# Kernel optimization log

Measured on AMD Instinct MI355X. Metric: run time of the kernel, lower is better.

## Reference

```python
import jax, jax.numpy as jnp
import numpy as np

N = 50000      # nodes
DEG = 16       # avg degree
E = N * DEG    # edges
FIN = 128
FQK = 64
FV = 64
H = 8


def setup_inputs() -> dict:
    key = jax.random.key(0)
    k1, k2, k3, k4 = jax.random.split(key, 4)
    x = jax.random.normal(k1, (N, FIN), dtype=jnp.float32)
    # torch Linear(Fin, 2*Fqk+Fv, bias=False); stored here as [Fin, Ftot] so y = x @ W
    W = jax.random.normal(k2, (FIN, 2 * FQK + FV), dtype=jnp.float32) / np.sqrt(FIN)
    # edges: src sorted and covering all nodes (required by scatter_softmax semantics)
    src = jnp.repeat(jnp.arange(N, dtype=jnp.int32), DEG)
    dest = jax.random.randint(k3, (E,), 0, N, dtype=jnp.int32)
    ei = jnp.stack([src, dest])  # [2, E]
    batch = jnp.sort(jax.random.randint(k4, (N,), 0, 64, dtype=jnp.int32))
    return {"x": x, "W": W, "batch": batch, "ei": ei}


def reference(x, W, batch, ei):
    n = x.shape[0]
    Fh = FQK // H   # per-head qk dim
    Fhv = FV // H   # per-head v dim
    scaling = float(Fh) ** (-0.5)

    qkv = x @ W  # [N, 2*Fqk+Fv]
    q, k, v = jnp.split(qkv, [FQK, 2 * FQK], axis=-1)
    q = (q * scaling).reshape(n, H, Fh)
    k = k.reshape(n, H, Fh)
    v = v.reshape(n, H, Fhv)

    src, dest = ei[0], ei[1]
    qs = q[src]   # [E, H, Fh]
    ks = k[dest]  # [E, H, Fh]
    vs = v[dest]  # [E, H, Fhv]

    aw = jnp.einsum("ehf,ehf->eh", qs, ks)  # per-edge per-head logits

    # segment softmax over src (numerically stable, same math as exp/segsum(exp))
    amax = jax.ops.segment_max(aw, src, num_segments=n)
    ex = jnp.exp(aw - amax[src])
    denom = jax.ops.segment_sum(ex, src, num_segments=n)
    aw = ex / denom[src]  # [E, H]

    out = jax.ops.segment_sum(aw[:, :, None] * vs, src, num_segments=n)  # [N, H, Fhv]
    return out.reshape(n, H * Fhv)
```

## Files before the change

### kernel.cpp

```cpp
#include <hip/hip_runtime.h>
#include <math.h>

#define N_NODES 50000
#define DEG 16
#define E_EDGES (N_NODES * DEG)
#define FIN 128
#define FTOT 192
#define FQK 64
#define FV 64
#define H 8

typedef __attribute__((ext_vector_type(8))) short short8;
typedef __attribute__((ext_vector_type(4))) float float4v;

__device__ inline unsigned short f2bf(float f) {
    unsigned int u = __float_as_uint(f);
    unsigned int r = u + 0x7fffu + ((u >> 16) & 1u);
    return (unsigned short)(r >> 16);
}

#define LDC 194

__global__ __launch_bounds__(256) void wprep(const float* __restrict__ W,
                                             unsigned short* __restrict__ Wb) {
    const int t = blockIdx.x * 256 + threadIdx.x;
    const int n = t % 192, kg = t / 192;
    unsigned short tmp[8];
#pragma unroll
    for (int j = 0; j < 8; j++)
        tmp[j] = f2bf(W[(kg * 8 + j) * FTOT + n]);
    *(uint4*)(Wb + n * FIN + kg * 8) = *(const uint4*)tmp;
}

__global__ __launch_bounds__(256) void gemm_qkv(const float* __restrict__ x,
                                                const unsigned short* __restrict__ Wb,
                                                unsigned short* __restrict__ qkv) {
    __shared__ unsigned short Bt[FTOT * FIN];
    unsigned short* Ct = Bt;
    const int tid = threadIdx.x;
    const int wave = tid >> 6, lane = tid & 63;
    const int m = lane & 15, q = lane >> 4;
    const int row = blockIdx.x * 64 + wave * 16 + m;
    const int rowc = min(row, N_NODES - 1);

    short8 a[4];
    const float* xr = x + (size_t)rowc * FIN;
#pragma unroll
    for (int s = 0; s < 4; s++) {
        float4v f0 = *(const float4v*)(xr + s * 32 + q * 8);
        float4v f1 = *(const float4v*)(xr + s * 32 + q * 8 + 4);
        short8 av;
        av[0] = (short)f2bf(f0.x); av[1] = (short)f2bf(f0.y);
        av[2] = (short)f2bf(f0.z); av[3] = (short)f2bf(f0.w);
        av[4] = (short)f2bf(f1.x); av[5] = (short)f2bf(f1.y);
        av[6] = (short)f2bf(f1.z); av[7] = (short)f2bf(f1.w);
        a[s] = av;
    }

#pragma unroll
    for (int i = 0; i < 12; i++) {
        const int c = i * 256 + tid;
        uint4 v = *(const uint4*)(Wb + c * 8);
        const int cs = c ^ ((c >> 4) & 7);
        *(uint4*)(&Bt[cs * 8]) = v;
    }
    __syncthreads();

    float4v acc[12];
#pragma unroll
    for (int ct = 0; ct < 12; ct++) acc[ct] = (float4v){0.f, 0.f, 0.f, 0.f};
#pragma unroll
    for (int ct = 0; ct < 12; ct++) {
        const int n = ct * 16 + m;
        const int sw = (n & 7) << 4;
#pragma unroll
        for (int s = 0; s < 4; s++) {
            const short8 b = *(const short8*)((const char*)Bt +
                             (((n << 8) + s * 64 + q * 16) ^ sw));
            acc[ct] = __builtin_amdgcn_mfma_f32_16x16x32_bf16(a[s], b, acc[ct], 0, 0, 0);
        }
    }
    __syncthreads();

    const int lrow0 = wave * 16 + q * 4;
#pragma unroll
    for (int ct = 0; ct < 12; ct++) {
        const int col = ct * 16 + m;
        int off; float scale;
        if (col < FQK)          { off = col;                      scale = 0.35355339059327373f; }
        else if (col < 2 * FQK) { off = 64 + 2 * (col - 64);      scale = 1.f; }
        else                    { off = 64 + 2 * (col - 128) + 1; scale = 1.f; }
#pragma unroll
        for (int i = 0; i < 4; i++)
            Ct[(lrow0 + i) * LDC + off] = f2bf(acc[ct][i] * scale);
    }
    __syncthreads();

    unsigned int* qg = (unsigned int*)qkv;
    const int base = blockIdx.x * 64;
#pragma unroll
    for (int i = 0; i < 24; i++) {
        int l = tid + i * 256;
        int r = l / 96, dw = l - r * 96;
        if (base + r < N_NODES)
            qg[(size_t)(base + r) * 96 + dw] = *(const unsigned int*)(&Ct[r * LDC + 2 * dw]);
    }
}

__global__ __launch_bounds__(256) void attn(const unsigned short* __restrict__ qkv,
                                            const int* __restrict__ dest,
                                            float* __restrict__ out) {
    const int node = blockIdx.x * 4 + (threadIdx.x >> 6);
    const int lane = threadIdx.x & 63;
    const int g = lane >> 2;
    const int r = lane & 3;
    if (node >= N_NODES) return;

    const int d = dest[node * DEG + g];

    const unsigned short* qp = qkv + (size_t)node * FTOT + 16 * r;
    const uint4 qv0 = *(const uint4*)(qp);
    const uint4 qv1 = *(const uint4*)(qp + 8);

    const unsigned short* kp = qkv + (size_t)d * FTOT + 64 + 32 * r;
    const uint4 kv0 = *(const uint4*)(kp);
    const uint4 kv1 = *(const uint4*)(kp + 8);
    const uint4 kv2 = *(const uint4*)(kp + 16);
    const uint4 kv3 = *(const uint4*)(kp + 24);

    const unsigned int qw[8]  = {qv0.x, qv0.y, qv0.z, qv0.w, qv1.x, qv1.y, qv1.z, qv1.w};
    const unsigned int kvw[16] = {kv0.x, kv0.y, kv0.z, kv0.w, kv1.x, kv1.y, kv1.z, kv1.w,
                                  kv2.x, kv2.y, kv2.z, kv2.w, kv3.x, kv3.y, kv3.z, kv3.w};

    float la = 0.f, lb = 0.f;
#pragma unroll
    for (int f = 0; f < 8; f++) {
        const unsigned int qa = qw[f >> 1];
        const unsigned int qb = qw[(f + 8) >> 1];
        const float qfa = __uint_as_float((f & 1) ? (qa & 0xffff0000u) : (qa << 16));
        const float qfb = __uint_as_float((f & 1) ? (qb & 0xffff0000u) : (qb << 16));
        la = fmaf(qfa, __uint_as_float(kvw[f] << 16), la);
        lb = fmaf(qfb, __uint_as_float(kvw[f + 8] << 16), lb);
    }

    float ma = la, mb = lb;
    ma = fmaxf(ma, __shfl_xor(ma, 4, 64));  mb = fmaxf(mb, __shfl_xor(mb, 4, 64));
    ma = fmaxf(ma, __shfl_xor(ma, 8, 64));  mb = fmaxf(mb, __shfl_xor(mb, 8, 64));
    ma = fmaxf(ma, __shfl_xor(ma, 16, 64)); mb = fmaxf(mb, __shfl_xor(mb, 16, 64));
    ma = fmaxf(ma, __shfl_xor(ma, 32, 64)); mb = fmaxf(mb, __shfl_xor(mb, 32, 64));
    const float pa = __expf(la - ma);
    const float pb = __expf(lb - mb);
    float sa = pa, sb = pb;
    sa += __shfl_xor(sa, 4, 64);  sb += __shfl_xor(sb, 4, 64);
    sa += __shfl_xor(sa, 8, 64);  sb += __shfl_xor(sb, 8, 64);
    sa += __shfl_xor(sa, 16, 64); sb += __shfl_xor(sb, 16, 64);
    sa += __shfl_xor(sa, 32, 64); sb += __shfl_xor(sb, 32, 64);

    float o[16];
#pragma unroll
    for (int w = 0; w < 8; w++) {
        o[w]     = pa * __uint_as_float(kvw[w] & 0xffff0000u);
        o[w + 8] = pb * __uint_as_float(kvw[w + 8] & 0xffff0000u);
    }
    {
        const bool up = (lane & 4) != 0;
#pragma unroll
        for (int j = 0; j < 8; j++) {
            const float send = up ? o[j] : o[j + 8];
            const float recv = __shfl_xor(send, 4, 64);
            o[j] = (up ? o[j + 8] : o[j]) + recv;
        }
    }
    {
        const bool up = (lane & 8) != 0;
#pragma unroll
        for (int j = 0; j < 4; j++) {
            const float send = up ? o[j] : o[j + 4];
            const float recv = __shfl_xor(send, 8, 64);
            o[j] = (up ? o[j + 4] : o[j]) + recv;
        }
    }
    {
        const bool up = (lane & 16) != 0;
#pragma unroll
        for (int j = 0; j < 2; j++) {
            const float send = up ? o[j] : o[j + 2];
            const float recv = __shfl_xor(send, 16, 64);
            o[j] = (up ? o[j + 2] : o[j]) + recv;
        }
    }
    {
        const bool up = (lane & 32) != 0;
        const float send = up ? o[0] : o[1];
        const float recv = __shfl_xor(send, 32, 64);
        o[0] = (up ? o[1] : o[0]) + recv;
    }
    const int w = ((g & 1) << 3) | ((g & 2) << 1) | ((g & 4) >> 1) | ((g & 8) >> 3);
    out[(size_t)node * 64 + 16 * r + w] = o[0] / ((w < 8) ? sa : sb);
}

extern "C" void kernel_launch(void* const* d_in, const int* in_sizes, int n_in,
                              void* d_out, int out_size, void* d_ws, size_t ws_size,
                              hipStream_t stream) {
    const float* x = (const float*)d_in[0];
    const float* W = (const float*)d_in[1];
    const int* ei = (const int*)d_in[3];
    const int* dest = ei + E_EDGES;
    float* out = (float*)d_out;

    unsigned short* qkv = (unsigned short*)d_ws;
    unsigned short* Wb  = qkv + (size_t)N_NODES * FTOT;

    wprep<<<12, 256, 0, stream>>>(W, Wb);
    gemm_qkv<<<(N_NODES + 63) / 64, 256, 0, stream>>>(x, Wb, qkv);
    attn<<<(N_NODES + 3) / 4, 256, 0, stream>>>(qkv, dest, out);
}
```

Before: 113.2 us.

## Fuse weight prep, QKV GEMM and attention into one persistent kernel with grid barrier

Merges the three kernels into one launch of 782 blocks. Each block converts W to bf16 in two halves directly into a smaller LDS buffer, computes its 64-row QKV tile, then waits at a global atomic barrier before running attention over 64 nodes per block with software prefetch of the next node's dest index and q. This removes two launch gaps and the separate W-prep pass, and cuts LDS use so more blocks fit per CU. The cost is that every block redoes the W conversion from fp32 global memory, and a spin barrier that relies on all 782 blocks being resident at once.

```diff
diff --git a/kernel.cpp b/kernel.cpp
--- a/kernel.cpp
+++ b/kernel.cpp
@@ -9,6 +9,7 @@
 #define FQK 64
 #define FV 64
 #define H 8
+#define NBLK 782
 
 typedef __attribute__((ext_vector_type(8))) short short8;
 typedef __attribute__((ext_vector_type(4))) float float4v;
@@ -21,182 +22,206 @@
 
 #define LDC 194
 
-__global__ __launch_bounds__(256) void wprep(const float* __restrict__ W,
-                                             unsigned short* __restrict__ Wb) {
-    const int t = blockIdx.x * 256 + threadIdx.x;
-    const int n = t % 192, kg = t / 192;
-    unsigned short tmp[8];
-#pragma unroll
-    for (int j = 0; j < 8; j++)
-        tmp[j] = f2bf(W[(kg * 8 + j) * FTOT + n]);
-    *(uint4*)(Wb + n * FIN + kg * 8) = *(const uint4*)tmp;
-}
-
-__global__ __launch_bounds__(256) void gemm_qkv(const float* __restrict__ x,
-                                                const unsigned short* __restrict__ Wb,
-                                                unsigned short* __restrict__ qkv) {
-    __shared__ unsigned short Bt[FTOT * FIN];
-    unsigned short* Ct = Bt;
+__global__ __launch_bounds__(256, 4) void fused(const float* __restrict__ x,
+                                                const float* __restrict__ W,
+                                                const int* __restrict__ dest,
+                                                unsigned short* __restrict__ qkv,
+                                                unsigned int* __restrict__ bar,
+                                                float* __restrict__ out) {
+    __shared__ unsigned short Bt[12544];
     const int tid = threadIdx.x;
     const int wave = tid >> 6, lane = tid & 63;
-    const int m = lane & 15, q = lane >> 4;
-    const int row = blockIdx.x * 64 + wave * 16 + m;
-    const int rowc = min(row, N_NODES - 1);
-
-    short8 a[4];
-    const float* xr = x + (size_t)rowc * FIN;
-#pragma unroll
-    for (int s = 0; s < 4; s++) {
-        float4v f0 = *(const float4v*)(xr + s * 32 + q * 8);
-        float4v f1 = *(const float4v*)(xr + s * 32 + q * 8 + 4);
-        short8 av;
-        av[0] = (short)f2bf(f0.x); av[1] = (short)f2bf(f0.y);
-        av[2] = (short)f2bf(f0.z); av[3] = (short)f2bf(f0.w);
-        av[4] = (short)f2bf(f1.x); av[5] = (short)f2bf(f1.y);
-        av[6] = (short)f2bf(f1.z); av[7] = (short)f2bf(f1.w);
-        a[s] = av;
+
+    {
+        const int m = lane & 15, q = lane >> 4;
+        const int row = blockIdx.x * 64 + wave * 16 + m;
+        const int rowc = min(row, N_NODES - 1);
+
+        short8 a[4];
+        const float* xr = x + (size_t)rowc * FIN;
+#pragma unroll
+        for (int s = 0; s < 4; s++) {
+            float4v f0 = *(const float4v*)(xr + s * 32 + q * 8);
+            float4v f1 = *(const float4v*)(xr + s * 32 + q * 8 + 4);
+            short8 av;
+            av[0] = (short)f2bf(f0.x); av[1] = (short)f2bf(f0.y);
+            av[2] = (short)f2bf(f0.z); av[3] = (short)f2bf(f0.w);
+            av[4] = (short)f2bf(f1.x); av[5] = (short)f2bf(f1.y);
+            av[6] = (short)f2bf(f1.z); av[7] = (short)f2bf(f1.w);
+            a[s] = av;
+        }
+
+        float4v acc[12];
+#pragma unroll
+        for (int ct = 0; ct < 12; ct++) acc[ct] = (float4v){0.f, 0.f, 0.f, 0.f};
+
+#pragma unroll
+        for (int h = 0; h < 2; h++) {
+#pragma unroll
+            for (int i = 0; i < 6; i++) {
+                const int c = i * 256 + tid;
+                const int n = c % 96, kg = c / 96;
+                unsigned short tmp[8];
+#pragma unroll
+                for (int j = 0; j < 8; j++)
+                    tmp[j] = f2bf(W[(kg * 8 + j) * FTOT + h * 96 + n]);
+                const int cs = (n * 16 + kg) ^ (n & 7);
+                *(uint4*)(&Bt[cs * 8]) = *(const uint4*)tmp;
+            }
+            __syncthreads();
+#pragma unroll
+            for (int j = 0; j < 6; j++) {
+                const int nl = j * 16 + m;
+                const int sw = (nl & 7) << 4;
+#pragma unroll
+                for (int s = 0; s < 4; s++) {
+                    const short8 b = *(const short8*)((const char*)Bt +
+                                     (((nl << 8) + s * 64 + q * 16) ^ sw));
+                    acc[h * 6 + j] =
+                        __builtin_amdgcn_mfma_f32_16x16x32_bf16(a[s], b, acc[h * 6 + j], 0, 0, 0);
+                }
+            }
+            __syncthreads();
+        }
+
+        unsigned short* Ct = Bt;
+        const int lrow0 = wave * 16 + q * 4;
+#pragma unroll
+        for (int ct = 0; ct < 12; ct++) {
+            const int col = ct * 16 + m;
+            int off; float scale;
+            if (col < FQK)          { off = col;                      scale = 0.35355339059327373f; }
+            else if (col < 2 * FQK) { off = 64 + 2 * (col - 64);      scale = 1.f; }
+            else                    { off = 64 + 2 * (col - 128) + 1; scale = 1.f; }
+#pragma unroll
+            for (int i = 0; i < 4; i++)
+                Ct[(lrow0 + i) * LDC + off] = f2bf(acc[ct][i] * scale);
+        }
+        __syncthreads();
+
+        unsigned int* qg = (unsigned int*)qkv;
+        const int base = blockIdx.x * 64;
+#pragma unroll
+        for (int i = 0; i < 24; i++) {
+            int l = tid + i * 256;
+            int r = l / 96, dw = l - r * 96;
+            if (base + r < N_NODES)
+                qg[(size_t)(base + r) * 96 + dw] = *(const unsigned int*)(&Ct[r * LDC + 2 * dw]);
+        }
     }
 
-#pragma unroll
-    for (int i = 0; i < 12; i++) {
-        const int c = i * 256 + tid;
-        uint4 v = *(const uint4*)(Wb + c * 8);
-        const int cs = c ^ ((c >> 4) & 7);
-        *(uint4*)(&Bt[cs * 8]) = v;
+    __threadfence();
+    if (tid == 0) {
+        __hip_atomic_fetch_add(bar, 1u, __ATOMIC_RELAXED, __HIP_MEMORY_SCOPE_AGENT);
+        while (__hip_atomic_load(bar, __ATOMIC_RELAXED, __HIP_MEMORY_SCOPE_AGENT) < NBLK)
+            __builtin_amdgcn_s_sleep(1);
     }
     __syncthreads();
-
-    float4v acc[12];
-#pragma unroll
-    for (int ct = 0; ct < 12; ct++) acc[ct] = (float4v){0.f, 0.f, 0.f, 0.f};
-#pragma unroll
-    for (int ct = 0; ct < 12; ct++) {
-        const int n = ct * 16 + m;
-        const int sw = (n & 7) << 4;
-#pragma unroll
-        for (int s = 0; s < 4; s++) {
-            const short8 b = *(const short8*)((const char*)Bt +
-                             (((n << 8) + s * 64 + q * 16) ^ sw));
-            acc[ct] = __builtin_amdgcn_mfma_f32_16x16x32_bf16(a[s], b, acc[ct], 0, 0, 0);
+    __threadfence();
+
+    {
+        const int g = lane >> 2;
+        const int r = lane & 3;
+        int node = blockIdx.x * 64 + wave;
+
+        int nodec = min(node, N_NODES - 1);
+        int d = dest[nodec * DEG + g];
+        const unsigned short* qp0 = qkv + (size_t)nodec * FTOT + 16 * r;
+        uint4 qv0 = *(const uint4*)(qp0);
+        uint4 qv1 = *(const uint4*)(qp0 + 8);
+
+#pragma unroll 1
+        for (int t = 0; t < 16; ++t) {
+            const unsigned short* kp = qkv + (size_t)d * FTOT + 64 + 32 * r;
+            const uint4 kv0 = *(const uint4*)(kp);
+            const uint4 kv1 = *(const uint4*)(kp + 8);
+            const uint4 kv2 = *(const uint4*)(kp + 16);
+            const uint4 kv3 = *(const uint4*)(kp + 24);
+
+            const int noden = node + 4;
+            int dN = d; uint4 nq0 = qv0, nq1 = qv1;
+            if (t < 15) {
+                const int nc = min(noden, N_NODES - 1);
+                dN = dest[nc * DEG + g];
+                const unsigned short* nqp = qkv + (size_t)nc * FTOT + 16 * r;
+                nq0 = *(const uint4*)(nqp);
+                nq1 = *(const uint4*)(nqp + 8);
+            }
+
+            const unsigned int qw[8]  = {qv0.x, qv0.y, qv0.z, qv0.w, qv1.x, qv1.y, qv1.z, qv1.w};
+            const unsigned int kvw[16] = {kv0.x, kv0.y, kv0.z, kv0.w, kv1.x, kv1.y, kv1.z, kv1.w,
+                                          kv2.x, kv2.y, kv2.z, kv2.w, kv3.x, kv3.y, kv3.z, kv3.w};
+
+            float la = 0.f, lb = 0.f;
+#pragma unroll
+            for (int f = 0; f < 8; f++) {
+                const unsigned int qa = qw[f >> 1];
+                const unsigned int qb = qw[(f + 8) >> 1];
+                const float qfa = __uint_as_float((f & 1) ? (qa & 0xffff0000u) : (qa << 16));
+                const float qfb = __uint_as_float((f & 1) ? (qb & 0xffff0000u) : (qb << 16));
+                la = fmaf(qfa, __uint_as_float(kvw[f] << 16), la);
+                lb = fmaf(qfb, __uint_as_float(kvw[f + 8] << 16), lb);
+            }
+
+            float ma = la, mb = lb;
+            ma = fmaxf(ma, __shfl_xor(ma, 4, 64));  mb = fmaxf(mb, __shfl_xor(mb, 4, 64));
+            ma = fmaxf(ma, __shfl_xor(ma, 8, 64));  mb = fmaxf(mb, __shfl_xor(mb, 8, 64));
+            ma = fmaxf(ma, __shfl_xor(ma, 16, 64)); mb = fmaxf(mb, __shfl_xor(mb, 16, 64));
+            ma = fmaxf(ma, __shfl_xor(ma, 32, 64)); mb = fmaxf(mb, __shfl_xor(mb, 32, 64));
+            const float pa = __expf(la - ma);
+            const float pb = __expf(lb - mb);
+            float sa = pa, sb = pb;
+            sa += __shfl_xor(sa, 4, 64);  sb += __shfl_xor(sb, 4, 64);
+            sa += __shfl_xor(sa, 8, 64);  sb += __shfl_xor(sb, 8, 64);
+            sa += __shfl_xor(sa, 16, 64); sb += __shfl_xor(sb, 16, 64);
+            sa += __shfl_xor(sa, 32, 64); sb += __shfl_xor(sb, 32, 64);
+
+            float o[16];
+#pragma unroll
+            for (int w = 0; w < 8; w++) {
+                o[w]     = pa * __uint_as_float(kvw[w] & 0xffff0000u);
+                o[w + 8] = pb * __uint_as_float(kvw[w + 8] & 0xffff0000u);
+            }
+            {
+                const bool up = (lane & 4) != 0;
+#pragma unroll
+                for (int j = 0; j < 8; j++) {
+                    const float send = up ? o[j] : o[j + 8];
+                    const float recv = __shfl_xor(send, 4, 64);
+                    o[j] = (up ? o[j + 8] : o[j]) + recv;
+                }
+            }
+            {
+                const bool up = (lane & 8) != 0;
+#pragma unroll
+                for (int j = 0; j < 4; j++) {
+                    const float send = up ? o[j] : o[j + 4];
+                    const float recv = __shfl_xor(send, 8, 64);
+                    o[j] = (up ? o[j + 4] : o[j]) + recv;
+                }
+            }
+            {
+                const bool up = (lane & 16) != 0;
+#pragma unroll
+                for (int j = 0; j < 2; j++) {
+                    const float send = up ? o[j] : o[j + 2];
+                    const float recv = __shfl_xor(send, 16, 64);
+                    o[j] = (up ? o[j + 2] : o[j]) + recv;
+                }
+            }
+            {
+                const bool up = (lane & 32) != 0;
+                const float send = up ? o[0] : o[1];
+                const float recv = __shfl_xor(send, 32, 64);
+                o[0] = (up ? o[1] : o[0]) + recv;
+            }
+            const int w = ((g & 1) << 3) | ((g & 2) << 1) | ((g & 4) >> 1) | ((g & 8) >> 3);
+            if (node < N_NODES)
+                out[(size_t)node * 64 + 16 * r + w] = o[0] / ((w < 8) ? sa : sb);
+
+            node = noden; d = dN; qv0 = nq0; qv1 = nq1;
         }
     }
-    __syncthreads();
-
-    const int lrow0 = wave * 16 + q * 4;
-#pragma unroll
-    for (int ct = 0; ct < 12; ct++) {
-        const int col = ct * 16 + m;
-        int off; float scale;
-        if (col < FQK)          { off = col;                      scale = 0.35355339059327373f; }
-        else if (col < 2 * FQK) { off = 64 + 2 * (col - 64);      scale = 1.f; }
-        else                    { off = 64 + 2 * (col - 128) + 1; scale = 1.f; }
-#pragma unroll
-        for (int i = 0; i < 4; i++)
-            Ct[(lrow0 + i) * LDC + off] = f2bf(acc[ct][i] * scale);
-    }
-    __syncthreads();
-
-    unsigned int* qg = (unsigned int*)qkv;
-    const int base = blockIdx.x * 64;
-#pragma unroll
-    for (int i = 0; i < 24; i++) {
-        int l = tid + i * 256;
-        int r = l / 96, dw = l - r * 96;
-        if (base + r < N_NODES)
-            qg[(size_t)(base + r) * 96 + dw] = *(const unsigned int*)(&Ct[r * LDC + 2 * dw]);
-    }
-}
-
-__global__ __launch_bounds__(256) void attn(const unsigned short* __restrict__ qkv,
-                                            const int* __restrict__ dest,
-                                            float* __restrict__ out) {
-    const int node = blockIdx.x * 4 + (threadIdx.x >> 6);
-    const int lane = threadIdx.x & 63;
-    const int g = lane >> 2;
-    const int r = lane & 3;
-    if (node >= N_NODES) return;
-
-    const int d = dest[node * DEG + g];
-
-    const unsigned short* qp = qkv + (size_t)node * FTOT + 16 * r;
-    const uint4 qv0 = *(const uint4*)(qp);
-    const uint4 qv1 = *(const uint4*)(qp + 8);
-
-    const unsigned short* kp = qkv + (size_t)d * FTOT + 64 + 32 * r;
-    const uint4 kv0 = *(const uint4*)(kp);
-    const uint4 kv1 = *(const uint4*)(kp + 8);
-    const uint4 kv2 = *(const uint4*)(kp + 16);
-    const uint4 kv3 = *(const uint4*)(kp + 24);
-
-    const unsigned int qw[8]  = {qv0.x, qv0.y, qv0.z, qv0.w, qv1.x, qv1.y, qv1.z, qv1.w};
-    const unsigned int kvw[16] = {kv0.x, kv0.y, kv0.z, kv0.w, kv1.x, kv1.y, kv1.z, kv1.w,
-                                  kv2.x, kv2.y, kv2.z, kv2.w, kv3.x, kv3.y, kv3.z, kv3.w};
-
-    float la = 0.f, lb = 0.f;
-#pragma unroll
-    for (int f = 0; f < 8; f++) {
-        const unsigned int qa = qw[f >> 1];
-        const unsigned int qb = qw[(f + 8) >> 1];
-        const float qfa = __uint_as_float((f & 1) ? (qa & 0xffff0000u) : (qa << 16));
-        const float qfb = __uint_as_float((f & 1) ? (qb & 0xffff0000u) : (qb << 16));
-        la = fmaf(qfa, __uint_as_float(kvw[f] << 16), la);
-        lb = fmaf(qfb, __uint_as_float(kvw[f + 8] << 16), lb);
-    }
-
-    float ma = la, mb = lb;
-    ma = fmaxf(ma, __shfl_xor(ma, 4, 64));  mb = fmaxf(mb, __shfl_xor(mb, 4, 64));
-    ma = fmaxf(ma, __shfl_xor(ma, 8, 64));  mb = fmaxf(mb, __shfl_xor(mb, 8, 64));
-    ma = fmaxf(ma, __shfl_xor(ma, 16, 64)); mb = fmaxf(mb, __shfl_xor(mb, 16, 64));
-    ma = fmaxf(ma, __shfl_xor(ma, 32, 64)); mb = fmaxf(mb, __shfl_xor(mb, 32, 64));
-    const float pa = __expf(la - ma);
-    const float pb = __expf(lb - mb);
-    float sa = pa, sb = pb;
-    sa += __shfl_xor(sa, 4, 64);  sb += __shfl_xor(sb, 4, 64);
-    sa += __shfl_xor(sa, 8, 64);  sb += __shfl_xor(sb, 8, 64);
-    sa += __shfl_xor(sa, 16, 64); sb += __shfl_xor(sb, 16, 64);
-    sa += __shfl_xor(sa, 32, 64); sb += __shfl_xor(sb, 32, 64);
-
-    float o[16];
-#pragma unroll
-    for (int w = 0; w < 8; w++) {
-        o[w]     = pa * __uint_as_float(kvw[w] & 0xffff0000u);
-        o[w + 8] = pb * __uint_as_float(kvw[w + 8] & 0xffff0000u);
-    }
-    {
-        const bool up = (lane & 4) != 0;
-#pragma unroll
-        for (int j = 0; j < 8; j++) {
-            const float send = up ? o[j] : o[j + 8];
-            const float recv = __shfl_xor(send, 4, 64);
-            o[j] = (up ? o[j + 8] : o[j]) + recv;
-        }
-    }
-    {
-        const bool up = (lane & 8) != 0;
-#pragma unroll
-        for (int j = 0; j < 4; j++) {
-            const float send = up ? o[j] : o[j + 4];
-            const float recv = __shfl_xor(send, 8, 64);
-            o[j] = (up ? o[j + 4] : o[j]) + recv;
-        }
-    }
-    {
-        const bool up = (lane & 16) != 0;
-#pragma unroll
-        for (int j = 0; j < 2; j++) {
-            const float send = up ? o[j] : o[j + 2];
-            const float recv = __shfl_xor(send, 16, 64);
-            o[j] = (up ? o[j + 2] : o[j]) + recv;
-        }
-    }
-    {
-        const bool up = (lane & 32) != 0;
-        const float send = up ? o[0] : o[1];
-        const float recv = __shfl_xor(send, 32, 64);
-        o[0] = (up ? o[1] : o[0]) + recv;
-    }
-    const int w = ((g & 1) << 3) | ((g & 2) << 1) | ((g & 4) >> 1) | ((g & 8) >> 3);
-    out[(size_t)node * 64 + 16 * r + w] = o[0] / ((w < 8) ? sa : sb);
 }
 
 extern "C" void kernel_launch(void* const* d_in, const int* in_sizes, int n_in,
@@ -209,9 +234,8 @@
     float* out = (float*)d_out;
 
     unsigned short* qkv = (unsigned short*)d_ws;
-    unsigned short* Wb  = qkv + (size_t)N_NODES * FTOT;
-
-    wprep<<<12, 256, 0, stream>>>(W, Wb);
-    gemm_qkv<<<(N_NODES + 63) / 64, 256, 0, stream>>>(x, Wb, qkv);
-    attn<<<(N_NODES + 3) / 4, 256, 0, stream>>>(qkv, dest, out);
+    unsigned int* bar = (unsigned int*)((char*)d_ws + (size_t)N_NODES * FTOT * 2);
+
+    hipMemsetAsync(bar, 0, 4, stream);
+    fused<<<NBLK, 256, 0, stream>>>(x, W, dest, qkv, bar, out);
 }
```

Measured after the change: 282.7 us. 2.5x slower.
